# Optimization experiments

Measured on AMD Instinct MI355X. Metric: run time of the kernel, lower is better.

The kernel has to match this reference:

```python
import jax, jax.numpy as jnp
import numpy as np

IN_FEATURES_LS = (8, 16, 32, 64, 128)
OUT_FEATURES = 512
MAX_FEAT = max(IN_FEATURES_LS)


def setup_inputs() -> dict:
    key = jax.random.key(0)
    k_x, k_idx, k_w, k_b = jax.random.split(key, 4)
    B, S = 16, 2048
    x = jax.random.normal(k_x, (B, S, MAX_FEAT), dtype=jnp.float32)
    # actual patch size per token: sample an index into in_features_ls
    idx = jax.random.randint(k_idx, (B, S), 0, len(IN_FEATURES_LS))
    in_feat_size = jnp.array(IN_FEATURES_LS, dtype=jnp.int64)[idx]
    weight = jax.random.normal(k_w, (len(IN_FEATURES_LS), OUT_FEATURES, MAX_FEAT), dtype=jnp.float32) * 0.05
    bias = jax.random.normal(k_b, (len(IN_FEATURES_LS), OUT_FEATURES), dtype=jnp.float32) * 0.05
    return {"x": x, "in_feat_size": in_feat_size, "weight": weight, "bias": bias}


def reference(x, in_feat_size, weight, bias):
    sizes = jnp.asarray(IN_FEATURES_LS)                       # [K]
    # mask padding columns of each expert's weight: [K, max_feat]
    feat_mask = (jnp.arange(MAX_FEAT)[None, :] < sizes[:, None]).astype(x.dtype)
    w = weight * feat_mask[:, None, :]                        # [K, out, max_feat]
    # all K projections computed unconditionally (faithful to original)
    y = jnp.einsum('bsi,koi->bsko', x, w) + bias              # [B, S, K, out]
    sel = (in_feat_size[..., None] == sizes).astype(x.dtype)  # [B, S, K] one-hot
    return jnp.einsum('bsko,bsk->bso', y, sel)                # [B, S, out]
```

## Files before the change

### kernel.cpp

```cpp
#include <hip/hip_runtime.h>

#define NEXP 5
#define MAXF 128
#define NOUT 512
#define PERMOFF 64

typedef __attribute__((ext_vector_type(8))) short short8;
typedef __attribute__((ext_vector_type(4))) float floatx4;

__device__ __forceinline__ ushort f2bf(float f) {
    uint u = __float_as_uint(f);
    u += 0x7FFF + ((u >> 16) & 1);
    return (ushort)(u >> 16);
}


__global__ __launch_bounds__(256) void misl_prep(
    const int* __restrict__ feat, const float* __restrict__ w,
    int* __restrict__ ws, ushort* __restrict__ wb, int n, int nb) {
    const int tid = threadIdx.x;
    if ((int)blockIdx.x < nb) {
        __shared__ int lcnt[NEXP], lbase[NEXP];
        if (tid < NEXP) lcnt[tid] = 0;
        __syncthreads();
        const int t = blockIdx.x * 256 + tid;
        int e = 0, r = 0;
        if (t < n) {
            e = __ffs(feat[t]) - 4;
            r = atomicAdd(&lcnt[e], 1);
        }
        __syncthreads();
        if (tid < NEXP) lbase[tid] = atomicAdd(&ws[8 + tid], lcnt[tid]);
        __syncthreads();
        if (t < n) ws[PERMOFF + e * n + lbase[e] + r] = t;
    } else {
        const int idx = ((int)blockIdx.x - nb) * 256 + tid;
        const int lane = idx & 63, nb16 = (idx >> 6) & 31;
        const int s = (idx >> 11) & 3, e = idx >> 13;
        if (e < NEXP) {
            const int ncol = nb16 * 16 + (lane & 15);
            const int k0 = s * 32 + (lane >> 4) * 8;
            const int K = 8 << e;
            const float* wr = w + ((size_t)e * NOUT + ncol) * MAXF + k0;
            short8 v;
            #pragma unroll
            for (int j = 0; j < 8; ++j)
                v[j] = (short)((k0 + j < K) ? f2bf(wr[j]) : (ushort)0);
            *(short8*)(wb + (size_t)idx * 8) = v;
        }
    }
}

template <int NS>
__device__ __forceinline__ void mfma_run(
    const float* __restrict__ x, const ushort* __restrict__ wbe,
    const float* __restrict__ be, const int* __restrict__ tokp, int rem,
    int lane, int n_base, float* __restrict__ out) {
    const int t = lane & 15, q = lane >> 4;
    const int nb16 = n_base >> 4;
    short8 wf[NS][4];
    #pragma unroll
    for (int s = 0; s < NS; ++s)
        #pragma unroll
        for (int bi = 0; bi < 4; ++bi)
            wf[s][bi] = *(const short8*)(wbe + ((size_t)(s * 32 + nb16 + bi) * 64 + lane) * 8);
    const float* bp = be + n_base + q * 4;

    if (rem == 64) {
        int tokv[4];
        #pragma unroll
        for (int g = 0; g < 4; ++g) tokv[g] = tokp[g * 16 + t];
        #pragma unroll
        for (int g = 0; g < 4; ++g) {
            const float* xr = x + (size_t)tokv[g] * MAXF + q * 8;
            floatx4 acc[4];
            #pragma unroll
            for (int bi = 0; bi < 4; ++bi)
                acc[bi] = *(const floatx4*)(bp + bi * 16);
            #pragma unroll
            for (int s = 0; s < NS; ++s) {
                const float4 xa = *(const float4*)(xr + s * 32);
                const float4 xc = *(const float4*)(xr + s * 32 + 4);
                short8 af;
                af[0] = (short)f2bf(xa.x); af[1] = (short)f2bf(xa.y);
                af[2] = (short)f2bf(xa.z); af[3] = (short)f2bf(xa.w);
                af[4] = (short)f2bf(xc.x); af[5] = (short)f2bf(xc.y);
                af[6] = (short)f2bf(xc.z); af[7] = (short)f2bf(xc.w);
                #pragma unroll
                for (int bi = 0; bi < 4; ++bi)
                    acc[bi] = __builtin_amdgcn_mfma_f32_16x16x32_bf16(wf[s][bi], af, acc[bi], 0, 0, 0);
            }
            float* orow = out + (size_t)tokv[g] * NOUT + n_base + q * 4;
            #pragma unroll
            for (int bi = 0; bi < 4; ++bi)
                *(floatx4*)(orow + bi * 16) = acc[bi];
        }
    } else {
        const int trips = (rem + 15) >> 4;
        for (int g = 0; g < trips; ++g) {
            const int base = g * 16;
            const int lim = rem - base;
            const int idx = (t < lim) ? t : lim - 1;
            const int tokv = tokp[base + idx];
            const float* xr = x + (size_t)tokv * MAXF + q * 8;
            floatx4 acc[4];
            #pragma unroll
            for (int bi = 0; bi < 4; ++bi)
                acc[bi] = *(const floatx4*)(bp + bi * 16);
            #pragma unroll
            for (int s = 0; s < NS; ++s) {
                const float4 xa = *(const float4*)(xr + s * 32);
                const float4 xc = *(const float4*)(xr + s * 32 + 4);
                short8 af;
                af[0] = (short)f2bf(xa.x); af[1] = (short)f2bf(xa.y);
                af[2] = (short)f2bf(xa.z); af[3] = (short)f2bf(xa.w);
                af[4] = (short)f2bf(xc.x); af[5] = (short)f2bf(xc.y);
                af[6] = (short)f2bf(xc.z); af[7] = (short)f2bf(xc.w);
                #pragma unroll
                for (int bi = 0; bi < 4; ++bi)
                    acc[bi] = __builtin_amdgcn_mfma_f32_16x16x32_bf16(wf[s][bi], af, acc[bi], 0, 0, 0);
            }
            if (t < lim) {
                float* orow = out + (size_t)tokv * NOUT + n_base + q * 4;
                #pragma unroll
                for (int bi = 0; bi < 4; ++bi)
                    *(floatx4*)(orow + bi * 16) = acc[bi];
            }
        }
    }
}

__global__ __launch_bounds__(512) void misl_main(
    const float* __restrict__ x, const ushort* __restrict__ wb,
    const float* __restrict__ b, const int* __restrict__ ws,
    float* __restrict__ out, int n) {
    const int g = blockIdx.x;
    const int c[NEXP] = {ws[8], ws[9], ws[10], ws[11], ws[12]};

    int gb = 0, e = -1, lgs = 0;
    #pragma unroll
    for (int j = 0; j < NEXP; ++j) {
        const int ee = 4 - j;
        const int ng = (c[ee] + 63) >> 6;
        if (e < 0 && g < gb + ng) { e = ee; lgs = g - gb; }
        gb += ng;
    }
    if (e < 0) return;

    int rem = c[e] - lgs * 64;
    if (rem > 64) rem = 64;
    const int* tokp = ws + PERMOFF + e * n + lgs * 64;
    const int lane = threadIdx.x & 63;
    const int wave = threadIdx.x >> 6;
    const int n_base = wave * 64;
    const ushort* wbe = wb + (size_t)e * 4 * 32 * 64 * 8;
    const float* be = b + e * NOUT;

    switch (e) {
        case 0: mfma_run<1>(x, wbe, be, tokp, rem, lane, n_base, out); break;
        case 1: mfma_run<1>(x, wbe, be, tokp, rem, lane, n_base, out); break;
        case 2: mfma_run<1>(x, wbe, be, tokp, rem, lane, n_base, out); break;
        case 3: mfma_run<2>(x, wbe, be, tokp, rem, lane, n_base, out); break;
        case 4: mfma_run<4>(x, wbe, be, tokp, rem, lane, n_base, out); break;
    }
}

extern "C" void kernel_launch(void* const* d_in, const int* in_sizes, int n_in,
                              void* d_out, int out_size, void* d_ws, size_t ws_size,
                              hipStream_t stream) {
    const float* x    = (const float*)d_in[0];
    const int*   feat = (const int*)d_in[1];
    const float* w    = (const float*)d_in[2];
    const float* b    = (const float*)d_in[3];
    float* out = (float*)d_out;
    int*   ws  = (int*)d_ws;

    const int n  = in_sizes[1];
    const int nb = (n + 255) / 256;

    const size_t wb_off = (((size_t)(PERMOFF + (size_t)NEXP * n) * 4) + 255) & ~(size_t)255;
    ushort* wb = (ushort*)((char*)d_ws + wb_off);

    hipMemsetAsync(ws, 0, 64 * sizeof(int), stream);
    misl_prep<<<nb + 160, 256, 0, stream>>>(feat, w, ws, wb, n, nb);
    misl_main<<<(n + 63) / 64 + NEXP, 512, 0, stream>>>(x, wb, b, ws, out, n);
}
```

Measured before the change: 105.4 us.

## Switch main kernel to persistent grid-stride over 16-token tiles

Replaces the one-block-per-64-token-group mapping with a fixed 2048-block persistent grid that strides over 16-token tiles, ordered from the largest expert down. The aim is finer load balance and less tail waste across CUs. In exchange, the weight fragments are reloaded for every 16-token tile instead of once per 64 tokens, and the unrolled 4-group fast path is lost, which reduces memory-level parallelism per block.

Result: slower. 108.8 us (+3.2%).

```diff
diff --git a/kernel.cpp b/kernel.cpp
--- a/kernel.cpp
+++ b/kernel.cpp
@@ -52,9 +52,9 @@
 }
 
 template <int NS>
-__device__ __forceinline__ void mfma_run(
+__device__ __forceinline__ void mfma_trip(
     const float* __restrict__ x, const ushort* __restrict__ wbe,
-    const float* __restrict__ be, const int* __restrict__ tokp, int rem,
+    const float* __restrict__ be, const int* __restrict__ tokp, int lim,
     int lane, int n_base, float* __restrict__ out) {
     const int t = lane & 15, q = lane >> 4;
     const int nb16 = n_base >> 4;
@@ -66,67 +66,31 @@
             wf[s][bi] = *(const short8*)(wbe + ((size_t)(s * 32 + nb16 + bi) * 64 + lane) * 8);
     const float* bp = be + n_base + q * 4;
 
-    if (rem == 64) {
-        int tokv[4];
+    const int idx = (t < lim) ? t : lim - 1;
+    const int tokv = tokp[idx];
+    const float* xr = x + (size_t)tokv * MAXF + q * 8;
+    floatx4 acc[4];
+    #pragma unroll
+    for (int bi = 0; bi < 4; ++bi)
+        acc[bi] = *(const floatx4*)(bp + bi * 16);
+    #pragma unroll
+    for (int s = 0; s < NS; ++s) {
+        const float4 xa = *(const float4*)(xr + s * 32);
+        const float4 xc = *(const float4*)(xr + s * 32 + 4);
+        short8 af;
+        af[0] = (short)f2bf(xa.x); af[1] = (short)f2bf(xa.y);
+        af[2] = (short)f2bf(xa.z); af[3] = (short)f2bf(xa.w);
+        af[4] = (short)f2bf(xc.x); af[5] = (short)f2bf(xc.y);
+        af[6] = (short)f2bf(xc.z); af[7] = (short)f2bf(xc.w);
         #pragma unroll
-        for (int g = 0; g < 4; ++g) tokv[g] = tokp[g * 16 + t];
+        for (int bi = 0; bi < 4; ++bi)
+            acc[bi] = __builtin_amdgcn_mfma_f32_16x16x32_bf16(wf[s][bi], af, acc[bi], 0, 0, 0);
+    }
+    if (t < lim) {
+        float* orow = out + (size_t)tokv * NOUT + n_base + q * 4;
         #pragma unroll
-        for (int g = 0; g < 4; ++g) {
-            const float* xr = x + (size_t)tokv[g] * MAXF + q * 8;
-            floatx4 acc[4];
-            #pragma unroll
-            for (int bi = 0; bi < 4; ++bi)
-                acc[bi] = *(const floatx4*)(bp + bi * 16);
-            #pragma unroll
-            for (int s = 0; s < NS; ++s) {
-                const float4 xa = *(const float4*)(xr + s * 32);
-                const float4 xc = *(const float4*)(xr + s * 32 + 4);
-                short8 af;
-                af[0] = (short)f2bf(xa.x); af[1] = (short)f2bf(xa.y);
-                af[2] = (short)f2bf(xa.z); af[3] = (short)f2bf(xa.w);
-                af[4] = (short)f2bf(xc.x); af[5] = (short)f2bf(xc.y);
-                af[6] = (short)f2bf(xc.z); af[7] = (short)f2bf(xc.w);
-                #pragma unroll
-                for (int bi = 0; bi < 4; ++bi)
-                    acc[bi] = __builtin_amdgcn_mfma_f32_16x16x32_bf16(wf[s][bi], af, acc[bi], 0, 0, 0);
-            }
-            float* orow = out + (size_t)tokv[g] * NOUT + n_base + q * 4;
-            #pragma unroll
-            for (int bi = 0; bi < 4; ++bi)
-                *(floatx4*)(orow + bi * 16) = acc[bi];
-        }
-    } else {
-        const int trips = (rem + 15) >> 4;
-        for (int g = 0; g < trips; ++g) {
-            const int base = g * 16;
-            const int lim = rem - base;
-            const int idx = (t < lim) ? t : lim - 1;
-            const int tokv = tokp[base + idx];
-            const float* xr = x + (size_t)tokv * MAXF + q * 8;
-            floatx4 acc[4];
-            #pragma unroll
-            for (int bi = 0; bi < 4; ++bi)
-                acc[bi] = *(const floatx4*)(bp + bi * 16);
-            #pragma unroll
-            for (int s = 0; s < NS; ++s) {
-                const float4 xa = *(const float4*)(xr + s * 32);
-                const float4 xc = *(const float4*)(xr + s * 32 + 4);
-                short8 af;
-                af[0] = (short)f2bf(xa.x); af[1] = (short)f2bf(xa.y);
-                af[2] = (short)f2bf(xa.z); af[3] = (short)f2bf(xa.w);
-                af[4] = (short)f2bf(xc.x); af[5] = (short)f2bf(xc.y);
-                af[6] = (short)f2bf(xc.z); af[7] = (short)f2bf(xc.w);
-                #pragma unroll
-                for (int bi = 0; bi < 4; ++bi)
-                    acc[bi] = __builtin_amdgcn_mfma_f32_16x16x32_bf16(wf[s][bi], af, acc[bi], 0, 0, 0);
-            }
-            if (t < lim) {
-                float* orow = out + (size_t)tokv * NOUT + n_base + q * 4;
-                #pragma unroll
-                for (int bi = 0; bi < 4; ++bi)
-                    *(floatx4*)(orow + bi * 16) = acc[bi];
-            }
-        }
+        for (int bi = 0; bi < 4; ++bi)
+            *(floatx4*)(orow + bi * 16) = acc[bi];
     }
 }
 
@@ -134,34 +98,36 @@
     const float* __restrict__ x, const ushort* __restrict__ wb,
     const float* __restrict__ b, const int* __restrict__ ws,
     float* __restrict__ out, int n) {
-    const int g = blockIdx.x;
     const int c[NEXP] = {ws[8], ws[9], ws[10], ws[11], ws[12]};
+    int tb[NEXP + 1];
+    tb[0] = 0;
+    #pragma unroll
+    for (int j = 0; j < NEXP; ++j)
+        tb[j + 1] = tb[j] + ((c[4 - j] + 15) >> 4);
+    const int total = tb[NEXP];
 
-    int gb = 0, e = -1, lgs = 0;
-    #pragma unroll
-    for (int j = 0; j < NEXP; ++j) {
-        const int ee = 4 - j;
-        const int ng = (c[ee] + 63) >> 6;
-        if (e < 0 && g < gb + ng) { e = ee; lgs = g - gb; }
-        gb += ng;
-    }
-    if (e < 0) return;
+    const int lane = threadIdx.x & 63;
+    const int n_base = (threadIdx.x >> 6) * 64;
 
-    int rem = c[e] - lgs * 64;
-    if (rem > 64) rem = 64;
-    const int* tokp = ws + PERMOFF + e * n + lgs * 64;
-    const int lane = threadIdx.x & 63;
-    const int wave = threadIdx.x >> 6;
-    const int n_base = wave * 64;
-    const ushort* wbe = wb + (size_t)e * 4 * 32 * 64 * 8;
-    const float* be = b + e * NOUT;
-
-    switch (e) {
-        case 0: mfma_run<1>(x, wbe, be, tokp, rem, lane, n_base, out); break;
-        case 1: mfma_run<1>(x, wbe, be, tokp, rem, lane, n_base, out); break;
-        case 2: mfma_run<1>(x, wbe, be, tokp, rem, lane, n_base, out); break;
-        case 3: mfma_run<2>(x, wbe, be, tokp, rem, lane, n_base, out); break;
-        case 4: mfma_run<4>(x, wbe, be, tokp, rem, lane, n_base, out); break;
+    for (int tr = blockIdx.x; tr < total; tr += gridDim.x) {
+        int j = 0;
+        #pragma unroll
+        for (int i = 0; i < NEXP - 1; ++i)
+            if (tr >= tb[i + 1]) j = i + 1;
+        const int e = 4 - j;
+        const int lt = tr - tb[j];
+        int lim = c[e] - lt * 16;
+        if (lim > 16) lim = 16;
+        const int* tokp = ws + PERMOFF + e * n + lt * 16;
+        const ushort* wbe = wb + (size_t)e * 4 * 32 * 64 * 8;
+        const float* be = b + e * NOUT;
+        switch (e) {
+            case 0: mfma_trip<1>(x, wbe, be, tokp, lim, lane, n_base, out); break;
+            case 1: mfma_trip<1>(x, wbe, be, tokp, lim, lane, n_base, out); break;
+            case 2: mfma_trip<1>(x, wbe, be, tokp, lim, lane, n_base, out); break;
+            case 3: mfma_trip<2>(x, wbe, be, tokp, lim, lane, n_base, out); break;
+            case 4: mfma_trip<4>(x, wbe, be, tokp, lim, lane, n_base, out); break;
+        }
     }
 }
 
@@ -183,5 +149,5 @@
 
     hipMemsetAsync(ws, 0, 64 * sizeof(int), stream);
     misl_prep<<<nb + 160, 256, 0, stream>>>(feat, w, ws, wb, n, nb);
-    misl_main<<<(n + 63) / 64 + NEXP, 512, 0, stream>>>(x, wb, b, ws, out, n);
+    misl_main<<<2048, 512, 0, stream>>>(x, wb, b, ws, out, n);
 }
```
